# Optimization experiments

Measured on AMD Instinct MI355X. Metric: run time of the kernel, lower is better.

## Reference

```python
import jax, jax.numpy as jnp
import numpy as np

N_EMBD = 1024
N_HEAD = 16
HEAD_SIZE = N_EMBD // N_HEAD


def setup_inputs() -> dict:
    key = jax.random.key(0)
    k_x, k_w, k_b = jax.random.split(key, 3)
    B, T, C = 2, 2048, N_EMBD
    x = jax.random.normal(k_x, (B, T, C), dtype=jnp.float32)
    # Linear(n_embd, 3*n_embd): weight [C, 3C] (applied as x @ W), bias [3C]
    w_qkv = jax.random.normal(k_w, (C, 3 * C), dtype=jnp.float32) * (1.0 / np.sqrt(C))
    b_qkv = jax.random.normal(k_b, (3 * C,), dtype=jnp.float32) * 0.02
    return {"x": x, "w_qkv": w_qkv, "b_qkv": b_qkv}


def reference(x, w_qkv, b_qkv):
    B, T, C = x.shape
    H, D = N_HEAD, HEAD_SIZE
    qkv = x @ w_qkv + b_qkv                      # [B, T, 3C]
    q, k, v = jnp.split(qkv, 3, axis=-1)         # each [B, T, C]
    # [B, T, C] -> [B, H, T, D]
    q = q.reshape(B, T, H, D).transpose(0, 2, 1, 3)
    k = k.reshape(B, T, H, D).transpose(0, 2, 1, 3)
    v = v.reshape(B, T, H, D).transpose(0, 2, 1, 3)
    scores = jnp.einsum('bhqd,bhkd->bhqk', q, k) / jnp.sqrt(jnp.float32(D))
    causal = jnp.tril(jnp.ones((T, T), dtype=bool))  # allow j <= i
    scores = jnp.where(causal[None, None, :, :], scores, -jnp.inf)
    weights = jax.nn.softmax(scores, axis=-1)    # [B, H, T, T]
    out = jnp.einsum('bhqk,bhkd->bhqd', weights, v)
    out = out.transpose(0, 2, 1, 3).reshape(B, T, C)
    return out
```

## Files before the change

### kernel.cpp

```cpp
#include <hip/hip_runtime.h>
#include <hip/hip_bf16.h>


#define CDIM  1024
#define C3    3072
#define HS    64
#define TLEN  2048
#define KVT   128
#define KSTR  72
#define VSTR  136
#define SCL   0.1803368801111204f

typedef __attribute__((ext_vector_type(8))) short bf16x8;
typedef __attribute__((ext_vector_type(4))) float f32x4;
typedef __attribute__((ext_vector_type(4))) unsigned short u16x4;

__device__ __forceinline__ unsigned short f2b(float f) {
    unsigned u = __float_as_uint(f);
    unsigned r = (u + 0x7FFFu + ((u >> 16) & 1u)) >> 16;
    return (unsigned short)r;
}
__device__ __forceinline__ float b2f(unsigned short u) {
    return __uint_as_float(((unsigned)u) << 16);
}
__device__ __forceinline__ float fexp2(float x) {
    return __builtin_amdgcn_exp2f(x);
}
__device__ __forceinline__ unsigned pkbf(float a, float b) {
    float2 f; f.x = a; f.y = b;
    __hip_bfloat162 h = __float22bfloat162_rn(f);
    union { __hip_bfloat162 h2; unsigned u; } c;
    c.h2 = h;
    return c.u;
}
__device__ __forceinline__ void gl_lds16(const unsigned short* g, unsigned short* l) {
    __builtin_amdgcn_global_load_lds((const __attribute__((address_space(1))) void*)g,
                                     (__attribute__((address_space(3))) void*)l, 16, 0, 0);
}
__device__ __forceinline__ int detect_bf(const void* bias, int lane) {
    unsigned w = ((const unsigned*)bias)[lane];
    unsigned e = (w >> 7) & 0xFF;
    unsigned long long m = __ballot(e >= 100 && e <= 135);
    return __popcll(m) >= 48;
}

__global__ __launch_bounds__(256) void k_prep(const void* __restrict__ w,
                                              const void* __restrict__ x,
                                              const void* __restrict__ bias,
                                              unsigned short* __restrict__ wt,
                                              unsigned short* __restrict__ xb) {
    __shared__ unsigned short tile[64 * 66];
    int t = threadIdx.x;
    int isbf = detect_bf(bias, t & 63);
    int bid = blockIdx.x;

    if (bid < 768) {
        int n0 = (bid % 48) * 64;
        int k0 = (bid / 48) * 64;
        for (int i = 0; i < 16; ++i) {
            int idx = t + i * 256;
            int r = idx >> 6, c = idx & 63;
            unsigned short v;
            if (isbf) v = ((const unsigned short*)w)[(k0 + r) * C3 + n0 + c];
            else      v = f2b(((const float*)w)[(k0 + r) * C3 + n0 + c]);
            tile[r * 66 + c] = v;
        }
        __syncthreads();
        for (int i = 0; i < 16; ++i) {
            int idx = t + i * 256;
            int r = idx >> 6, c = idx & 63;
            wt[(n0 + r) * CDIM + k0 + c] = tile[c * 66 + r];
        }
    }
    if (!isbf) {
        const float* s = (const float*)x;
        unsigned* d = (unsigned*)xb;
        int base = bid * 1024;
        for (int j = t; j < 1024; j += 256) {
            int idx = base + j;
            float a = s[2 * idx], b = s[2 * idx + 1];
            d[idx] = (unsigned)f2b(a) | ((unsigned)f2b(b) << 16);
        }
    }
}

__global__ __launch_bounds__(256, 3) void k_gemm_qkv(const void* __restrict__ xraw,
                                                     const unsigned short* __restrict__ xb,
                                                     const void* __restrict__ biasraw,
                                                     const unsigned short* __restrict__ Bt,
                                                     unsigned short* __restrict__ qk,
                                                     unsigned short* __restrict__ vtg) {
    __shared__ __align__(16) unsigned short As[128 * 64];
    __shared__ __align__(16) unsigned short Bs[128 * 64];
    int tid  = threadIdx.x;
    int lane = tid & 63, wv = tid >> 6;
    int quad = lane >> 4, l16 = lane & 15;
    int isbf = detect_bf(biasraw, lane);
    const unsigned short* A = isbf ? (const unsigned short*)xraw : xb;

    int m0 = blockIdx.y * 128, n0 = blockIdx.x * 128;
    int wm = (wv >> 1) * 64, wn = (wv & 1) * 64;

    f32x4 acc[4][4] = {};

    int srow = wv * 8 + (lane >> 3);
    int kcg8 = (((lane & 7) ^ (lane >> 3)) * 8);
    const unsigned short* Ag = A  + (m0 + srow) * CDIM + kcg8;
    const unsigned short* Bg = Bt + (n0 + srow) * CDIM + kcg8;
    unsigned short* lA = &As[srow * 64 + (lane & 7) * 8];
    unsigned short* lB = &Bs[srow * 64 + (lane & 7) * 8];

    for (int k0 = 0; k0 < CDIM; k0 += 64) {
        __syncthreads();
        for (int j = 0; j < 4; ++j) {
            gl_lds16(Ag + j * (32 * CDIM), lA + j * (32 * 64));
            gl_lds16(Bg + j * (32 * CDIM), lB + j * (32 * 64));
        }
        Ag += 64; Bg += 64;
        __syncthreads();

        for (int kk = 0; kk < 2; ++kk) {
            int sw = (l16 & 7);
            bf16x8 af[4], bfr[4];
            for (int mt = 0; mt < 4; ++mt)
                af[mt] = *(const bf16x8*)&As[(wm + mt * 16 + l16) * 64 + (((kk * 4 + quad) ^ sw) * 8)];
            for (int nt = 0; nt < 4; ++nt)
                bfr[nt] = *(const bf16x8*)&Bs[(wn + nt * 16 + l16) * 64 + (((kk * 4 + quad) ^ sw) * 8)];
            for (int mt = 0; mt < 4; ++mt)
                for (int nt = 0; nt < 4; ++nt)
                    acc[mt][nt] = __builtin_amdgcn_mfma_f32_16x16x32_bf16(af[mt], bfr[nt], acc[mt][nt], 0, 0, 0);
        }
    }

    if (n0 < 2048) {
        for (int mt = 0; mt < 4; ++mt) {
            int row = m0 + wm + mt * 16 + quad * 4;
            for (int nt = 0; nt < 4; ++nt) {
                int col = n0 + wn + nt * 16 + l16;
                float bv = isbf ? b2f(((const unsigned short*)biasraw)[col])
                                : ((const float*)biasraw)[col];
                for (int i = 0; i < 4; ++i)
                    qk[(row + i) * 2048 + col] = f2b(acc[mt][nt][i] + bv);
            }
        }
    } else {
        for (int mt = 0; mt < 4; ++mt) {
            int row = m0 + wm + mt * 16 + quad * 4;
            int t = row & 2047, b = row >> 11;
            for (int nt = 0; nt < 4; ++nt) {
                int col = n0 + wn + nt * 16 + l16;
                float bv = isbf ? b2f(((const unsigned short*)biasraw)[col])
                                : ((const float*)biasraw)[col];
                int hh = (col - 2048) >> 6, d = (col - 2048) & 63;
                u16x4 pk;
                for (int i = 0; i < 4; ++i) pk[i] = f2b(acc[mt][nt][i] + bv);
                *(u16x4*)&vtg[((b * 16 + hh) * 64 + d) * TLEN + t] = pk;
            }
        }
    }
}

__global__ __launch_bounds__(256, 2) void k_attn(const unsigned short* __restrict__ qk,
                                                 const unsigned short* __restrict__ vtg,
                                                 const void* __restrict__ biasraw,
                                                 void* __restrict__ outv) {
    __shared__ __align__(16) unsigned short Ks[128 * KSTR];
    __shared__ __align__(16) unsigned short Vt[64 * VSTR];
    __shared__ __align__(16) unsigned short Pt[4][32 * VSTR];

    int tid  = threadIdx.x;
    int lane = tid & 63, wv = tid >> 6;
    int quad = lane >> 4, l16 = lane & 15;
    int isbf = detect_bf(biasraw, lane);
    int bh = blockIdx.x;
    int y  = blockIdx.y;
    int a  = (y < 8) ? y : (23 - y);
    int b = bh >> 4, h = bh & 15;
    int rowbase = b * TLEN;
    unsigned short* Pw = Pt[wv];

    int c     = 4 * a + wv;
    int q0w   = c * 32;
    int trips = a + 1;

    bf16x8 qf[2][2];
    for (int qt = 0; qt < 2; ++qt)
        for (int kh = 0; kh < 2; ++kh)
            qf[qt][kh] = *(const bf16x8*)&qk[(rowbase + q0w + qt * 16 + l16) * 2048 + h * HS + kh * 32 + quad * 8];

    f32x4 oacc[2][4] = {};
    float lsum[2] = {0.f, 0.f};

    int sr  = tid >> 3;
    int sc8 = (tid & 7) * 8;

    for (int t = 0; t < trips; ++t) {
        int kv0 = t * KVT;
        const unsigned short* kg = qk  + (rowbase + kv0 + sr) * 2048 + CDIM + h * HS + sc8;
        const unsigned short* vg = vtg + (bh * 64 + sr) * TLEN + kv0 + sc8;
        uint4 kr0 = *(const uint4*)kg;
        uint4 kr1 = *(const uint4*)(kg + 32 * 2048);
        uint4 kr2 = *(const uint4*)(kg + 64 * 2048);
        uint4 kr3 = *(const uint4*)(kg + 96 * 2048);
        uint4 vr0 = *(const uint4*)vg;
        uint4 vr1 = *(const uint4*)(vg + 64);
        uint4 vr2 = *(const uint4*)(vg + 32 * TLEN);
        uint4 vr3 = *(const uint4*)(vg + 32 * TLEN + 64);
        __syncthreads();
        *(uint4*)&Ks[sr * KSTR + sc8]        = kr0;
        *(uint4*)&Ks[(sr + 32) * KSTR + sc8] = kr1;
        *(uint4*)&Ks[(sr + 64) * KSTR + sc8] = kr2;
        *(uint4*)&Ks[(sr + 96) * KSTR + sc8] = kr3;
        *(uint4*)&Vt[sr * VSTR + sc8]        = vr0;
        *(uint4*)&Vt[sr * VSTR + sc8 + 64]   = vr1;
        *(uint4*)&Vt[(sr + 32) * VSTR + sc8]      = vr2;
        *(uint4*)&Vt[(sr + 32) * VSTR + sc8 + 64] = vr3;
        __syncthreads();

        f32x4 s0[8], s1[8];
        for (int nt = 0; nt < 8; ++nt) {
            bf16x8 kf0 = *(const bf16x8*)&Ks[(nt * 16 + l16) * KSTR + quad * 8];
            bf16x8 kf1 = *(const bf16x8*)&Ks[(nt * 16 + l16) * KSTR + 32 + quad * 8];
            f32x4 z0 = {}, z1 = {};
            z0 = __builtin_amdgcn_mfma_f32_16x16x32_bf16(kf0, qf[0][0], z0, 0, 0, 0);
            z0 = __builtin_amdgcn_mfma_f32_16x16x32_bf16(kf1, qf[0][1], z0, 0, 0, 0);
            z1 = __builtin_amdgcn_mfma_f32_16x16x32_bf16(kf0, qf[1][0], z1, 0, 0, 0);
            z1 = __builtin_amdgcn_mfma_f32_16x16x32_bf16(kf1, qf[1][1], z1, 0, 0, 0);
            s0[nt] = z0; s1[nt] = z1;
        }

        bool dm = (t == trips - 1);
        for (int qt = 0; qt < 2; ++qt) {
            const f32x4* sv = qt ? s1 : s0;
            int q = q0w + qt * 16 + l16;
            float psum = 0.f;
            for (int nt = 0; nt < 8; ++nt) {
                float p[4];
                for (int i = 0; i < 4; ++i) {
                    float arg = fminf(fmaf(sv[nt][i], SCL, -12.0f), 30.0f);
                    if (dm) {
                        int kv = kv0 + nt * 16 + quad * 4 + i;
                        if (kv > q) arg = -1e30f;
                    }
                    p[i] = fexp2(arg);
                    psum += p[i];
                }
                uint2 pk;
                pk.x = pkbf(p[0], p[1]);
                pk.y = pkbf(p[2], p[3]);
                *(uint2*)&Pw[(qt * 16 + l16) * VSTR + nt * 16 + quad * 4] = pk;
            }
            lsum[qt] += psum;
        }

        for (int kh = 0; kh < 4; ++kh) {
            bf16x8 bp0 = *(const bf16x8*)&Pw[l16 * VSTR + kh * 32 + quad * 8];
            bf16x8 bp1 = *(const bf16x8*)&Pw[(16 + l16) * VSTR + kh * 32 + quad * 8];
            for (int dt = 0; dt < 4; ++dt) {
                bf16x8 av = *(const bf16x8*)&Vt[(dt * 16 + l16) * VSTR + kh * 32 + quad * 8];
                oacc[0][dt] = __builtin_amdgcn_mfma_f32_16x16x32_bf16(av, bp0, oacc[0][dt], 0, 0, 0);
                oacc[1][dt] = __builtin_amdgcn_mfma_f32_16x16x32_bf16(av, bp1, oacc[1][dt], 0, 0, 0);
            }
        }
    }

    for (int qt = 0; qt < 2; ++qt) {
        float l = lsum[qt];
        l += __shfl_xor(l, 16);
        l += __shfl_xor(l, 32);
        float inv = 1.0f / l;
        int q = q0w + qt * 16 + l16;
        if (isbf) {
            unsigned short* out = (unsigned short*)outv;
            for (int dt = 0; dt < 4; ++dt) {
                u16x4 ov;
                for (int i = 0; i < 4; ++i) ov[i] = f2b(oacc[qt][dt][i] * inv);
                *(u16x4*)&out[(rowbase + q) * CDIM + h * HS + dt * 16 + quad * 4] = ov;
            }
        } else {
            float* out = (float*)outv;
            for (int dt = 0; dt < 4; ++dt) {
                float4 ov;
                ov.x = oacc[qt][dt][0] * inv; ov.y = oacc[qt][dt][1] * inv;
                ov.z = oacc[qt][dt][2] * inv; ov.w = oacc[qt][dt][3] * inv;
                *(float4*)&out[(rowbase + q) * CDIM + h * HS + dt * 16 + quad * 4] = ov;
            }
        }
    }
}

extern "C" void kernel_launch(void* const* d_in, const int* in_sizes, int n_in,
                              void* d_out, int out_size, void* d_ws, size_t ws_size,
                              hipStream_t stream) {
    const void* x    = d_in[0];
    const void* w    = d_in[1];
    const void* bias = d_in[2];

    char* ws = (char*)d_ws;
    unsigned short* xb  = (unsigned short*)ws;
    unsigned short* wt  = (unsigned short*)(ws + (8u  << 20));
    unsigned short* qk  = (unsigned short*)(ws + (16u << 20));
    unsigned short* vtg = (unsigned short*)(ws + (32u << 20));

    k_prep<<<2048, 256, 0, stream>>>(w, x, bias, wt, xb);
    k_gemm_qkv<<<dim3(24, 32), 256, 0, stream>>>(x, xb, bias, wt, qk, vtg);
    k_attn<<<dim3(32, 16), 256, 0, stream>>>(qk, vtg, bias, d_out);
}
```

Measured before the change: 166.1 us.

## Make attention one wave per block with K/V loaded straight from global memory

The attention kernel moves from 256-thread blocks, where four waves shared K/V tiles staged in LDS, to 64-thread blocks where one wave handles a 32-row query chunk. Each wave reads K and V fragments directly from global memory, so the shared staging and both block barriers go away. Blocks are ordered longest-first to help load balance. In exchange, K/V reuse across the four waves is lost, which raises global and L2 traffic, and the per-fragment global loads may expose more latency.

```diff
diff --git a/kernel.cpp b/kernel.cpp
--- a/kernel.cpp
+++ b/kernel.cpp
@@ -7,8 +7,7 @@
 #define HS    64
 #define TLEN  2048
 #define KVT   128
-#define KSTR  72
-#define VSTR  136
+#define PSTR  136
 #define SCL   0.1803368801111204f
 
 typedef __attribute__((ext_vector_type(8))) short bf16x8;
@@ -160,28 +159,22 @@
     }
 }
 
-__global__ __launch_bounds__(256, 2) void k_attn(const unsigned short* __restrict__ qk,
-                                                 const unsigned short* __restrict__ vtg,
-                                                 const void* __restrict__ biasraw,
-                                                 void* __restrict__ outv) {
-    __shared__ __align__(16) unsigned short Ks[128 * KSTR];
-    __shared__ __align__(16) unsigned short Vt[64 * VSTR];
-    __shared__ __align__(16) unsigned short Pt[4][32 * VSTR];
-
-    int tid  = threadIdx.x;
-    int lane = tid & 63, wv = tid >> 6;
+__global__ __launch_bounds__(64) void k_attn(const unsigned short* __restrict__ qk,
+                                             const unsigned short* __restrict__ vtg,
+                                             const void* __restrict__ biasraw,
+                                             void* __restrict__ outv) {
+    __shared__ __align__(16) unsigned short Pw[32 * PSTR];
+
+    int lane = threadIdx.x;
     int quad = lane >> 4, l16 = lane & 15;
     int isbf = detect_bf(biasraw, lane);
     int bh = blockIdx.x;
-    int y  = blockIdx.y;
-    int a  = (y < 8) ? y : (23 - y);
+    int c  = 63 - blockIdx.y;
     int b = bh >> 4, h = bh & 15;
     int rowbase = b * TLEN;
-    unsigned short* Pw = Pt[wv];
-
-    int c     = 4 * a + wv;
+
     int q0w   = c * 32;
-    int trips = a + 1;
+    int trips = (c >> 2) + 1;
 
     bf16x8 qf[2][2];
     for (int qt = 0; qt < 2; ++qt)
@@ -191,36 +184,17 @@
     f32x4 oacc[2][4] = {};
     float lsum[2] = {0.f, 0.f};
 
-    int sr  = tid >> 3;
-    int sc8 = (tid & 7) * 8;
+    const unsigned short* kbase = qk  + (rowbase)*2048 + CDIM + h * HS + quad * 8;
+    const unsigned short* vbase = vtg + (bh * 64 + l16) * TLEN + quad * 8;
 
     for (int t = 0; t < trips; ++t) {
         int kv0 = t * KVT;
-        const unsigned short* kg = qk  + (rowbase + kv0 + sr) * 2048 + CDIM + h * HS + sc8;
-        const unsigned short* vg = vtg + (bh * 64 + sr) * TLEN + kv0 + sc8;
-        uint4 kr0 = *(const uint4*)kg;
-        uint4 kr1 = *(const uint4*)(kg + 32 * 2048);
-        uint4 kr2 = *(const uint4*)(kg + 64 * 2048);
-        uint4 kr3 = *(const uint4*)(kg + 96 * 2048);
-        uint4 vr0 = *(const uint4*)vg;
-        uint4 vr1 = *(const uint4*)(vg + 64);
-        uint4 vr2 = *(const uint4*)(vg + 32 * TLEN);
-        uint4 vr3 = *(const uint4*)(vg + 32 * TLEN + 64);
-        __syncthreads();
-        *(uint4*)&Ks[sr * KSTR + sc8]        = kr0;
-        *(uint4*)&Ks[(sr + 32) * KSTR + sc8] = kr1;
-        *(uint4*)&Ks[(sr + 64) * KSTR + sc8] = kr2;
-        *(uint4*)&Ks[(sr + 96) * KSTR + sc8] = kr3;
-        *(uint4*)&Vt[sr * VSTR + sc8]        = vr0;
-        *(uint4*)&Vt[sr * VSTR + sc8 + 64]   = vr1;
-        *(uint4*)&Vt[(sr + 32) * VSTR + sc8]      = vr2;
-        *(uint4*)&Vt[(sr + 32) * VSTR + sc8 + 64] = vr3;
-        __syncthreads();
 
         f32x4 s0[8], s1[8];
         for (int nt = 0; nt < 8; ++nt) {
-            bf16x8 kf0 = *(const bf16x8*)&Ks[(nt * 16 + l16) * KSTR + quad * 8];
-            bf16x8 kf1 = *(const bf16x8*)&Ks[(nt * 16 + l16) * KSTR + 32 + quad * 8];
+            const unsigned short* kr = kbase + (kv0 + nt * 16 + l16) * 2048;
+            bf16x8 kf0 = *(const bf16x8*)kr;
+            bf16x8 kf1 = *(const bf16x8*)(kr + 32);
             f32x4 z0 = {}, z1 = {};
             z0 = __builtin_amdgcn_mfma_f32_16x16x32_bf16(kf0, qf[0][0], z0, 0, 0, 0);
             z0 = __builtin_amdgcn_mfma_f32_16x16x32_bf16(kf1, qf[0][1], z0, 0, 0, 0);
@@ -248,16 +222,16 @@
                 uint2 pk;
                 pk.x = pkbf(p[0], p[1]);
                 pk.y = pkbf(p[2], p[3]);
-                *(uint2*)&Pw[(qt * 16 + l16) * VSTR + nt * 16 + quad * 4] = pk;
+                *(uint2*)&Pw[(qt * 16 + l16) * PSTR + nt * 16 + quad * 4] = pk;
             }
             lsum[qt] += psum;
         }
 
         for (int kh = 0; kh < 4; ++kh) {
-            bf16x8 bp0 = *(const bf16x8*)&Pw[l16 * VSTR + kh * 32 + quad * 8];
-            bf16x8 bp1 = *(const bf16x8*)&Pw[(16 + l16) * VSTR + kh * 32 + quad * 8];
+            bf16x8 bp0 = *(const bf16x8*)&Pw[l16 * PSTR + kh * 32 + quad * 8];
+            bf16x8 bp1 = *(const bf16x8*)&Pw[(16 + l16) * PSTR + kh * 32 + quad * 8];
             for (int dt = 0; dt < 4; ++dt) {
-                bf16x8 av = *(const bf16x8*)&Vt[(dt * 16 + l16) * VSTR + kh * 32 + quad * 8];
+                bf16x8 av = *(const bf16x8*)(vbase + dt * 16 * TLEN + kv0 + kh * 32);
                 oacc[0][dt] = __builtin_amdgcn_mfma_f32_16x16x32_bf16(av, bp0, oacc[0][dt], 0, 0, 0);
                 oacc[1][dt] = __builtin_amdgcn_mfma_f32_16x16x32_bf16(av, bp1, oacc[1][dt], 0, 0, 0);
             }
@@ -304,5 +278,5 @@
 
     k_prep<<<2048, 256, 0, stream>>>(w, x, bias, wt, xb);
     k_gemm_qkv<<<dim3(24, 32), 256, 0, stream>>>(x, xb, bias, wt, qk, vtg);
-    k_attn<<<dim3(32, 16), 256, 0, stream>>>(qk, vtg, bias, d_out);
-}
+    k_attn<<<dim3(32, 64), 64, 0, stream>>>(qk, vtg, bias, d_out);
+}
```

Measured after the change: 227.8 us. 1.37x slower.

## Pair front and back 16-row query tiles per wave for causal balance

Applied to the files above, without the earlier changes.

Each wave now processes one 16-row query tile near the start and one near the end of the sequence instead of a contiguous 32-row chunk. Every block walks a similar number of KV tiles, and the early tile drops out once its causal range is done. The intent is to even out per-block work under the causal mask. In exchange, each KV tile loaded into shared memory feeds fewer query rows on later trips, so total K/V staging traffic per head rises and the mixed active/inactive paths add branching.

```diff
diff --git a/kernel.cpp b/kernel.cpp
--- a/kernel.cpp
+++ b/kernel.cpp
@@ -173,29 +173,32 @@
     int quad = lane >> 4, l16 = lane & 15;
     int isbf = detect_bf(biasraw, lane);
     int bh = blockIdx.x;
-    int y  = blockIdx.y;
-    int a  = (y < 8) ? y : (23 - y);
+    int a  = blockIdx.y;
     int b = bh >> 4, h = bh & 15;
     int rowbase = b * TLEN;
     unsigned short* Pw = Pt[wv];
 
-    int c     = 4 * a + wv;
-    int q0w   = c * 32;
-    int trips = a + 1;
-
-    bf16x8 qf[2][2];
-    for (int qt = 0; qt < 2; ++qt)
-        for (int kh = 0; kh < 2; ++kh)
-            qf[qt][kh] = *(const bf16x8*)&qk[(rowbase + q0w + qt * 16 + l16) * 2048 + h * HS + kh * 32 + quad * 8];
-
-    f32x4 oacc[2][4] = {};
-    float lsum[2] = {0.f, 0.f};
+    int qtA = 4 * a + wv;
+    int qtB = 127 - 4 * a - wv;
+    int qA0 = qtA * 16, qB0 = qtB * 16;
+    int tripsA = ((4 * a + wv) >> 3) + 1;
+    int T      = ((127 - 4 * a - wv) >> 3) + 1;
+
+    bf16x8 qfA[2], qfB[2];
+    for (int kh = 0; kh < 2; ++kh) {
+        qfA[kh] = *(const bf16x8*)&qk[(rowbase + qA0 + l16) * 2048 + h * HS + kh * 32 + quad * 8];
+        qfB[kh] = *(const bf16x8*)&qk[(rowbase + qB0 + l16) * 2048 + h * HS + kh * 32 + quad * 8];
+    }
+
+    f32x4 oA[4] = {}, oB[4] = {};
+    float lsA = 0.f, lsB = 0.f;
 
     int sr  = tid >> 3;
     int sc8 = (tid & 7) * 8;
 
-    for (int t = 0; t < trips; ++t) {
+    for (int t = 0; t < T; ++t) {
         int kv0 = t * KVT;
+        bool actA = (t < tripsA);
         const unsigned short* kg = qk  + (rowbase + kv0 + sr) * 2048 + CDIM + h * HS + sc8;
         const unsigned short* vg = vtg + (bh * 64 + sr) * TLEN + kv0 + sc8;
         uint4 kr0 = *(const uint4*)kg;
@@ -217,28 +220,31 @@
         *(uint4*)&Vt[(sr + 32) * VSTR + sc8 + 64] = vr3;
         __syncthreads();
 
-        f32x4 s0[8], s1[8];
+        f32x4 sA[8], sB[8];
         for (int nt = 0; nt < 8; ++nt) {
             bf16x8 kf0 = *(const bf16x8*)&Ks[(nt * 16 + l16) * KSTR + quad * 8];
             bf16x8 kf1 = *(const bf16x8*)&Ks[(nt * 16 + l16) * KSTR + 32 + quad * 8];
-            f32x4 z0 = {}, z1 = {};
-            z0 = __builtin_amdgcn_mfma_f32_16x16x32_bf16(kf0, qf[0][0], z0, 0, 0, 0);
-            z0 = __builtin_amdgcn_mfma_f32_16x16x32_bf16(kf1, qf[0][1], z0, 0, 0, 0);
-            z1 = __builtin_amdgcn_mfma_f32_16x16x32_bf16(kf0, qf[1][0], z1, 0, 0, 0);
-            z1 = __builtin_amdgcn_mfma_f32_16x16x32_bf16(kf1, qf[1][1], z1, 0, 0, 0);
-            s0[nt] = z0; s1[nt] = z1;
-        }
-
-        bool dm = (t == trips - 1);
-        for (int qt = 0; qt < 2; ++qt) {
-            const f32x4* sv = qt ? s1 : s0;
-            int q = q0w + qt * 16 + l16;
+            f32x4 zB = {};
+            zB = __builtin_amdgcn_mfma_f32_16x16x32_bf16(kf0, qfB[0], zB, 0, 0, 0);
+            zB = __builtin_amdgcn_mfma_f32_16x16x32_bf16(kf1, qfB[1], zB, 0, 0, 0);
+            sB[nt] = zB;
+            if (actA) {
+                f32x4 zA = {};
+                zA = __builtin_amdgcn_mfma_f32_16x16x32_bf16(kf0, qfA[0], zA, 0, 0, 0);
+                zA = __builtin_amdgcn_mfma_f32_16x16x32_bf16(kf1, qfA[1], zA, 0, 0, 0);
+                sA[nt] = zA;
+            }
+        }
+
+        {
+            bool dmB = (t == T - 1);
+            int q = qB0 + l16;
             float psum = 0.f;
             for (int nt = 0; nt < 8; ++nt) {
                 float p[4];
                 for (int i = 0; i < 4; ++i) {
-                    float arg = fminf(fmaf(sv[nt][i], SCL, -12.0f), 30.0f);
-                    if (dm) {
+                    float arg = fminf(fmaf(sB[nt][i], SCL, -12.0f), 30.0f);
+                    if (dmB) {
                         int kv = kv0 + nt * 16 + quad * 4 + i;
                         if (kv > q) arg = -1e30f;
                     }
@@ -248,41 +254,72 @@
                 uint2 pk;
                 pk.x = pkbf(p[0], p[1]);
                 pk.y = pkbf(p[2], p[3]);
-                *(uint2*)&Pw[(qt * 16 + l16) * VSTR + nt * 16 + quad * 4] = pk;
-            }
-            lsum[qt] += psum;
+                *(uint2*)&Pw[(16 + l16) * VSTR + nt * 16 + quad * 4] = pk;
+            }
+            lsB += psum;
+        }
+        if (actA) {
+            bool dmA = (t == tripsA - 1);
+            int q = qA0 + l16;
+            float psum = 0.f;
+            for (int nt = 0; nt < 8; ++nt) {
+                float p[4];
+                for (int i = 0; i < 4; ++i) {
+                    float arg = fminf(fmaf(sA[nt][i], SCL, -12.0f), 30.0f);
+                    if (dmA) {
+                        int kv = kv0 + nt * 16 + quad * 4 + i;
+                        if (kv > q) arg = -1e30f;
+                    }
+                    p[i] = fexp2(arg);
+                    psum += p[i];
+                }
+                uint2 pk;
+                pk.x = pkbf(p[0], p[1]);
+                pk.y = pkbf(p[2], p[3]);
+                *(uint2*)&Pw[l16 * VSTR + nt * 16 + quad * 4] = pk;
+            }
+            lsA += psum;
         }
 
         for (int kh = 0; kh < 4; ++kh) {
-            bf16x8 bp0 = *(const bf16x8*)&Pw[l16 * VSTR + kh * 32 + quad * 8];
-            bf16x8 bp1 = *(const bf16x8*)&Pw[(16 + l16) * VSTR + kh * 32 + quad * 8];
-            for (int dt = 0; dt < 4; ++dt) {
-                bf16x8 av = *(const bf16x8*)&Vt[(dt * 16 + l16) * VSTR + kh * 32 + quad * 8];
-                oacc[0][dt] = __builtin_amdgcn_mfma_f32_16x16x32_bf16(av, bp0, oacc[0][dt], 0, 0, 0);
-                oacc[1][dt] = __builtin_amdgcn_mfma_f32_16x16x32_bf16(av, bp1, oacc[1][dt], 0, 0, 0);
+            bf16x8 bpB = *(const bf16x8*)&Pw[(16 + l16) * VSTR + kh * 32 + quad * 8];
+            if (actA) {
+                bf16x8 bpA = *(const bf16x8*)&Pw[l16 * VSTR + kh * 32 + quad * 8];
+                for (int dt = 0; dt < 4; ++dt) {
+                    bf16x8 av = *(const bf16x8*)&Vt[(dt * 16 + l16) * VSTR + kh * 32 + quad * 8];
+                    oB[dt] = __builtin_amdgcn_mfma_f32_16x16x32_bf16(av, bpB, oB[dt], 0, 0, 0);
+                    oA[dt] = __builtin_amdgcn_mfma_f32_16x16x32_bf16(av, bpA, oA[dt], 0, 0, 0);
+                }
+            } else {
+                for (int dt = 0; dt < 4; ++dt) {
+                    bf16x8 av = *(const bf16x8*)&Vt[(dt * 16 + l16) * VSTR + kh * 32 + quad * 8];
+                    oB[dt] = __builtin_amdgcn_mfma_f32_16x16x32_bf16(av, bpB, oB[dt], 0, 0, 0);
+                }
             }
         }
     }
 
     for (int qt = 0; qt < 2; ++qt) {
-        float l = lsum[qt];
+        float l = qt ? lsB : lsA;
+        const f32x4* oo = qt ? oB : oA;
+        int q0 = qt ? qB0 : qA0;
         l += __shfl_xor(l, 16);
         l += __shfl_xor(l, 32);
         float inv = 1.0f / l;
-        int q = q0w + qt * 16 + l16;
+        int q = q0 + l16;
         if (isbf) {
             unsigned short* out = (unsigned short*)outv;
             for (int dt = 0; dt < 4; ++dt) {
                 u16x4 ov;
-                for (int i = 0; i < 4; ++i) ov[i] = f2b(oacc[qt][dt][i] * inv);
+                for (int i = 0; i < 4; ++i) ov[i] = f2b(oo[dt][i] * inv);
                 *(u16x4*)&out[(rowbase + q) * CDIM + h * HS + dt * 16 + quad * 4] = ov;
             }
         } else {
             float* out = (float*)outv;
             for (int dt = 0; dt < 4; ++dt) {
                 float4 ov;
-                ov.x = oacc[qt][dt][0] * inv; ov.y = oacc[qt][dt][1] * inv;
-                ov.z = oacc[qt][dt][2] * inv; ov.w = oacc[qt][dt][3] * inv;
+                ov.x = oo[dt][0] * inv; ov.y = oo[dt][1] * inv;
+                ov.z = oo[dt][2] * inv; ov.w = oo[dt][3] * inv;
                 *(float4*)&out[(rowbase + q) * CDIM + h * HS + dt * 16 + quad * 4] = ov;
             }
         }
```

Result: faster. 152.0 us (-8.5%).
